# Kernel tuning notes

Measured on AMD Instinct MI355X. Metric: run time of the kernel, lower is better.

## Reference

```python
import jax, jax.numpy as jnp
import numpy as np
import math

N_HEADS = 16
D_EMBED = 1024
D_HEAD = D_EMBED // N_HEADS


def setup_inputs() -> dict:
    key = jax.random.key(0)
    ks = jax.random.split(key, 5)
    B, T = 4, 2048
    x = jax.random.normal(ks[0], (B, T, D_EMBED), dtype=jnp.float32)
    s_in = 1.0 / math.sqrt(D_EMBED)
    W_in = jax.random.normal(ks[1], (3 * D_EMBED, D_EMBED), dtype=jnp.float32) * s_in
    b_in = jax.random.normal(ks[2], (3 * D_EMBED,), dtype=jnp.float32) * s_in
    W_out = jax.random.normal(ks[3], (D_EMBED, D_EMBED), dtype=jnp.float32) * s_in
    b_out = jax.random.normal(ks[4], (D_EMBED,), dtype=jnp.float32) * s_in
    return {"x": x, "W_in": W_in, "b_in": b_in, "W_out": W_out, "b_out": b_out,
            "causal_mask": 1}


def reference(x, W_in, b_in, W_out, b_out, causal_mask):
    B, T, C = x.shape
    # in_proj: x @ W_in^T + b_in -> (B,T,3C), chunk into q,k,v
    qkv = jnp.einsum('btc,ec->bte', x, W_in) + b_in
    q, k, v = jnp.split(qkv, 3, axis=-1)
    # (B,T,H,Dh) -> (B,H,T,Dh)
    def heads(t):
        return t.reshape(B, T, N_HEADS, D_HEAD).transpose(0, 2, 1, 3)
    q, k, v = heads(q), heads(k), heads(v)
    scores = jnp.einsum('bhqd,bhkd->bhqk', q, k) / math.sqrt(D_HEAD)
    if causal_mask:
        mask = jnp.triu(jnp.ones((T, T), dtype=bool), k=1)  # True above diagonal
        scores = jnp.where(mask, -jnp.inf, scores)
    attn = jax.nn.softmax(scores, axis=-1)
    out = jnp.einsum('bhqk,bhkd->bhqd', attn, v)
    out = out.transpose(0, 2, 1, 3).reshape(B, T, C)
    out = jnp.einsum('btc,oc->bto', out, W_out) + b_out
    return out
```

## Files before the change

kernel.cpp:

```cpp
#include <hip/hip_runtime.h>
#include <hip/hip_bf16.h>

#define T_SEQ 2048
#define D_EMB 1024
#define NH    16
#define DH    64
#define NB    4
#define MROWS (NB * T_SEQ)
#define QKVN  (3 * D_EMB)

typedef __attribute__((ext_vector_type(8))) short bf16x8;
typedef __attribute__((ext_vector_type(4))) float f32x4;

__device__ __forceinline__ unsigned short f2bf(float f) {
  __hip_bfloat16 h = __float2bfloat16(f);
  return __builtin_bit_cast(unsigned short, h);
}

__device__ __forceinline__ void gload_lds16(const void* g, void* lds) {
  __builtin_amdgcn_global_load_lds(
      (const __attribute__((address_space(1))) void*)g,
      (__attribute__((address_space(3))) void*)lds, 16, 0, 0);
}

__global__ __launch_bounds__(256) void cvt_kernel(const float* __restrict__ in,
                                                  unsigned short* __restrict__ out,
                                                  int n4) {
  for (int i = blockIdx.x * 256 + threadIdx.x; i < n4; i += gridDim.x * 256) {
    const float4 v = reinterpret_cast<const float4*>(in)[i];
    ushort4 o;
    o.x = f2bf(v.x); o.y = f2bf(v.y); o.z = f2bf(v.z); o.w = f2bf(v.w);
    reinterpret_cast<ushort4*>(out)[i] = o;
  }
}

template <int OUT_BF16>
__global__ __launch_bounds__(256) void gemm_bt(const unsigned short* __restrict__ A,
                                               const unsigned short* __restrict__ Bt,
                                               const float* __restrict__ bias,
                                               void* __restrict__ Cout,
                                               int M, int N, int K) {
  __shared__ __align__(16) unsigned short As[128 * 32];
  __shared__ __align__(16) unsigned short Bs[128 * 32];

  const int tid = threadIdx.x;
  const int w  = tid >> 6;
  const int l  = tid & 63;
  const int lr = l & 15;
  const int lk = (l >> 4) * 8;
  const int bm = blockIdx.y * 128;
  const int bn = blockIdx.x * 128;
  const int wr = (w >> 1) * 64;
  const int wc = (w & 1) * 64;

  f32x4 acc[4][4];
#pragma unroll
  for (int i = 0; i < 4; ++i)
#pragma unroll
    for (int j = 0; j < 4; ++j) acc[i][j] = (f32x4){0.f, 0.f, 0.f, 0.f};

  const int srow = l >> 2;
  const int sk   = (l & 3) * 8;
  const unsigned short* Ab = A + (size_t)(bm + w * 32 + srow) * K + sk;
  const unsigned short* Bb = Bt + (size_t)(bn + w * 32 + srow) * K + sk;

  for (int kt = 0; kt < K; kt += 32) {
    gload_lds16(Ab + kt,                  &As[(w * 32 + 0) * 32]);
    gload_lds16(Ab + kt + (size_t)16 * K, &As[(w * 32 + 16) * 32]);
    gload_lds16(Bb + kt,                  &Bs[(w * 32 + 0) * 32]);
    gload_lds16(Bb + kt + (size_t)16 * K, &Bs[(w * 32 + 16) * 32]);
    __syncthreads();

    bf16x8 a[4], b[4];
#pragma unroll
    for (int mi = 0; mi < 4; ++mi)
      a[mi] = *reinterpret_cast<const bf16x8*>(&As[(wr + mi * 16 + lr) * 32 + lk]);
#pragma unroll
    for (int ni = 0; ni < 4; ++ni)
      b[ni] = *reinterpret_cast<const bf16x8*>(&Bs[(wc + ni * 16 + lr) * 32 + lk]);
#pragma unroll
    for (int mi = 0; mi < 4; ++mi)
#pragma unroll
      for (int ni = 0; ni < 4; ++ni)
        acc[mi][ni] = __builtin_amdgcn_mfma_f32_16x16x32_bf16(a[mi], b[ni], acc[mi][ni], 0, 0, 0);
    __syncthreads();
  }

  const int lg = l >> 4;
#pragma unroll
  for (int mi = 0; mi < 4; ++mi)
#pragma unroll
    for (int ni = 0; ni < 4; ++ni)
#pragma unroll
      for (int i = 0; i < 4; ++i) {
        const int row = bm + wr + mi * 16 + lg * 4 + i;
        const int col = bn + wc + ni * 16 + lr;
        const float v = acc[mi][ni][i] + bias[col];
        if (OUT_BF16)
          ((unsigned short*)Cout)[(size_t)row * N + col] = f2bf(v);
        else
          ((float*)Cout)[(size_t)row * N + col] = v;
      }
}

__global__ __launch_bounds__(512, 4) void attn_fwd(const unsigned short* __restrict__ qkv,
                                                   unsigned short* __restrict__ attn_out,
                                                   const int* __restrict__ causal_flag) {
  __shared__ __align__(16) unsigned short Ks[64 * 64];
  __shared__ __align__(16) unsigned short Vt[64 * 64];
  __shared__ __align__(16) unsigned short Ps[8][16 * 64];

  const int tid = threadIdx.x;
  const int w  = tid >> 6;
  const int l  = tid & 63;
  const int lr = l & 15;
  const int lg = l >> 4;
  const int lk = lg * 8;
  const int bx = blockIdx.x;
  const int bh = blockIdx.y;
  const int b  = bh >> 4;
  const int h  = bh & 15;
  const int causal = causal_flag[0];

  const unsigned short* Qp = qkv + (size_t)(b * T_SEQ) * QKVN + h * DH;
  const unsigned short* Kp = Qp + D_EMB;
  const unsigned short* Vp = Qp + 2 * D_EMB;

  for (int qq = 0; qq < 2; ++qq) {
    const int qt = qq ? (15 - bx) : bx;
    const int qbase = qt * 128;
    const int wrow0 = qbase + w * 16;

    bf16x8 qf[2];
#pragma unroll
    for (int ks = 0; ks < 2; ++ks) {
      bf16x8 v = *reinterpret_cast<const bf16x8*>(
          Qp + (size_t)(wrow0 + lr) * QKVN + ks * 32 + lk);
#pragma unroll
      for (int j = 0; j < 8; ++j) {
        const float f = __builtin_bit_cast(float, ((unsigned)(unsigned short)v[j]) << 16)
                        * 0.180336879f;
        v[j] = (short)(__builtin_bit_cast(unsigned, f) >> 16);
      }
      qf[ks] = v;
    }

    f32x4 oacc[4];
    float mrow = -INFINITY, lsum = 0.f;
#pragma unroll
    for (int di = 0; di < 4; ++di) oacc[di] = (f32x4){0.f, 0.f, 0.f, 0.f};

    const int nt = causal ? (qt * 2 + 2) : (T_SEQ / 64);

    for (int kb = 0; kb < nt; ++kb) {
      const int kbase = kb * 64;
      {
        const int cj = (l & 7) ^ (l >> 3);
        gload_lds16(Kp + (size_t)(kbase + w * 8 + (l >> 3)) * QKVN + cj * 8,
                    &Ks[(w * 8) * 64]);
      }
      {
        const int k  = tid & 63;
        const int d0 = (tid >> 6) * 8;
        bf16x8 v = *reinterpret_cast<const bf16x8*>(Vp + (size_t)(kbase + k) * QKVN + d0);
#pragma unroll
        for (int j = 0; j < 8; ++j)
          Vt[(d0 + j) * 64 + (k ^ (j << 3))] = ((unsigned short*)&v)[j];
      }
      __syncthreads();

      const bool live = !causal || (kbase <= wrow0 + 15);
      if (live) {
        f32x4 s[4];
#pragma unroll
        for (int ni = 0; ni < 4; ++ni) s[ni] = (f32x4){0.f, 0.f, 0.f, 0.f};
#pragma unroll
        for (int ks = 0; ks < 2; ++ks) {
          bf16x8 kf[4];
#pragma unroll
          for (int ni = 0; ni < 4; ++ni) {
            const int R = ni * 16 + lr;
            kf[ni] = *reinterpret_cast<const bf16x8*>(
                &Ks[R * 64 + (((ks * 4 + lg) ^ (lr & 7)) << 3)]);
          }
#pragma unroll
          for (int ni = 0; ni < 4; ++ni)
            s[ni] = __builtin_amdgcn_mfma_f32_16x16x32_bf16(kf[ni], qf[ks], s[ni], 0, 0, 0);
        }

        const bool mm = causal && (kbase + 63 > wrow0);
        const int qrow_rel = wrow0 + lr - kbase;
        float rmax = -INFINITY;
#pragma unroll
        for (int ni = 0; ni < 4; ++ni)
#pragma unroll
          for (int i = 0; i < 4; ++i) {
            float v = s[ni][i];
            if (mm && (ni * 16 + lg * 4 + i > qrow_rel)) v = -INFINITY;
            s[ni][i] = v;
            rmax = fmaxf(rmax, v);
          }
        rmax = fmaxf(rmax, __shfl_xor(rmax, 16));
        rmax = fmaxf(rmax, __shfl_xor(rmax, 32));
        const float mnew = fmaxf(mrow, rmax);
        const float alpha = exp2f(mrow - mnew);
        mrow = mnew;
        float psum = 0.f;
#pragma unroll
        for (int ni = 0; ni < 4; ++ni)
#pragma unroll
          for (int i = 0; i < 4; ++i) {
            const float p = exp2f(s[ni][i] - mnew);
            s[ni][i] = p;
            psum += p;
          }
        psum += __shfl_xor(psum, 16);
        psum += __shfl_xor(psum, 32);
        lsum = lsum * alpha + psum;

#pragma unroll
        for (int i = 0; i < 4; ++i) {
          const float a_bc = __shfl(alpha, (l & 48) | (lg * 4 + i));
#pragma unroll
          for (int di = 0; di < 4; ++di) oacc[di][i] *= a_bc;
        }

#pragma unroll
        for (int ni = 0; ni < 4; ++ni) {
          const unsigned lo = (unsigned)f2bf(s[ni][0]) | ((unsigned)f2bf(s[ni][1]) << 16);
          const unsigned hi = (unsigned)f2bf(s[ni][2]) | ((unsigned)f2bf(s[ni][3]) << 16);
          const int chunk = (ni * 2 + (lg >> 1)) ^ (lr & 7);
          uint2* dst = reinterpret_cast<uint2*>(
              reinterpret_cast<char*>(&Ps[w][0]) + lr * 128 + chunk * 16 + (lg & 1) * 8);
          *dst = make_uint2(lo, hi);
        }

#pragma unroll
        for (int ks2 = 0; ks2 < 2; ++ks2) {
          bf16x8 pf, vf[4];
          pf = *reinterpret_cast<const bf16x8*>(
              &Ps[w][lr * 64 + (((ks2 * 4 + lg) ^ (lr & 7)) << 3)]);
#pragma unroll
          for (int di = 0; di < 4; ++di) {
            const int R = di * 16 + lr;
            vf[di] = *reinterpret_cast<const bf16x8*>(
                &Vt[R * 64 + (((ks2 * 4 + lg) ^ (lr & 7)) << 3)]);
          }
#pragma unroll
          for (int di = 0; di < 4; ++di)
            oacc[di] = __builtin_amdgcn_mfma_f32_16x16x32_bf16(pf, vf[di], oacc[di], 0, 0, 0);
        }
      }
      __syncthreads();
    }

#pragma unroll
    for (int i = 0; i < 4; ++i) {
      const float ls = __shfl(lsum, (l & 48) | (lg * 4 + i));
      const float inv = 1.0f / ls;
#pragma unroll
      for (int di = 0; di < 4; ++di) {
        const int q = wrow0 + lg * 4 + i;
        const int d = di * 16 + lr;
        attn_out[(size_t)(b * T_SEQ + q) * D_EMB + h * DH + d] =
            f2bf(oacc[di][i] * inv);
      }
    }
  }
}

extern "C" void kernel_launch(void* const* d_in, const int* in_sizes, int n_in,
                              void* d_out, int out_size, void* d_ws, size_t ws_size,
                              hipStream_t stream) {
  const float* x     = (const float*)d_in[0];
  const float* W_in  = (const float*)d_in[1];
  const float* b_in  = (const float*)d_in[2];
  const float* W_out = (const float*)d_in[3];
  const float* b_out = (const float*)d_in[4];
  const int*   causal = (const int*)d_in[5];
  float* out = (float*)d_out;

  char* ws = (char*)d_ws;
  unsigned short* x_bf    = (unsigned short*)(ws);
  unsigned short* win_bf  = (unsigned short*)(ws + 16777216);
  unsigned short* wout_bf = (unsigned short*)(ws + 23068672);
  unsigned short* qkv     = (unsigned short*)(ws + 25165824);
  unsigned short* attn    = (unsigned short*)(ws + 75497472);

  cvt_kernel<<<2048, 256, 0, stream>>>(x, x_bf, (MROWS * D_EMB) / 4);
  cvt_kernel<<<2048, 256, 0, stream>>>(W_in, win_bf, (QKVN * D_EMB) / 4);
  cvt_kernel<<<1024, 256, 0, stream>>>(W_out, wout_bf, (D_EMB * D_EMB) / 4);

  gemm_bt<1><<<dim3(QKVN / 128, MROWS / 128), 256, 0, stream>>>(
      x_bf, win_bf, b_in, qkv, MROWS, QKVN, D_EMB);

  attn_fwd<<<dim3(8, NB * NH), 512, 0, stream>>>(qkv, attn, causal);

  gemm_bt<0><<<dim3(D_EMB / 128, MROWS / 128), 256, 0, stream>>>(
      attn, wout_bf, b_out, out, MROWS, D_EMB, D_EMB);
}
```

Measured before the change: 299.2 us.

## Pre-transpose V in a separate kernel and widen GEMM K-tile with swizzled LDS

Adds a transposeV kernel that writes V head-major and transposed into the workspace, so attention can stage V tiles with direct global-to-LDS loads instead of scalar transposing stores in its inner loop. The GEMM now uses a K-tile of 64 with XOR-swizzled LDS layout, which halves the number of barriers per K. It also remaps workgroups through a swizzle for better L2 locality. The trade-off is an extra kernel launch plus a round trip of V through memory, and twice the LDS per GEMM block.

```diff
diff --git a/kernel.cpp b/kernel.cpp
--- a/kernel.cpp
+++ b/kernel.cpp
@@ -34,22 +34,57 @@
   }
 }
 
+__global__ __launch_bounds__(256) void transposeV(const unsigned short* __restrict__ qkv,
+                                                  unsigned short* __restrict__ vt) {
+  __shared__ __align__(16) unsigned short Lt[64 * 72];
+  const int tid = threadIdx.x;
+  const int t0 = blockIdx.x * 64;
+  const int bh = blockIdx.y;
+  const int b  = bh >> 4;
+  const int h  = bh & 15;
+  const unsigned short* src = qkv + (size_t)(b * T_SEQ) * QKVN + 2 * D_EMB + h * DH;
+#pragma unroll
+  for (int g = 0; g < 2; ++g) {
+    const int r = (tid >> 3) + g * 32;
+    const int c = tid & 7;
+    bf16x8 v = *reinterpret_cast<const bf16x8*>(src + (size_t)(t0 + r) * QKVN + c * 8);
+    *reinterpret_cast<bf16x8*>(reinterpret_cast<char*>(Lt) + r * 144 + c * 16) = v;
+  }
+  __syncthreads();
+#pragma unroll
+  for (int g = 0; g < 2; ++g) {
+    const int d  = (tid >> 3) + g * 32;
+    const int tc = tid & 7;
+    bf16x8 o;
+#pragma unroll
+    for (int j = 0; j < 8; ++j)
+      ((unsigned short*)&o)[j] = Lt[(tc * 8 + j) * 72 + d];
+    *reinterpret_cast<bf16x8*>(vt + ((size_t)bh * 64 + d) * T_SEQ + t0 + tc * 8) = o;
+  }
+}
+
 template <int OUT_BF16>
 __global__ __launch_bounds__(256) void gemm_bt(const unsigned short* __restrict__ A,
                                                const unsigned short* __restrict__ Bt,
                                                const float* __restrict__ bias,
                                                void* __restrict__ Cout,
                                                int M, int N, int K) {
-  __shared__ __align__(16) unsigned short As[128 * 32];
-  __shared__ __align__(16) unsigned short Bs[128 * 32];
+  __shared__ __align__(16) unsigned short As[128 * 64];
+  __shared__ __align__(16) unsigned short Bs[128 * 64];
 
   const int tid = threadIdx.x;
   const int w  = tid >> 6;
   const int l  = tid & 63;
   const int lr = l & 15;
-  const int lk = (l >> 4) * 8;
-  const int bm = blockIdx.y * 128;
-  const int bn = blockIdx.x * 128;
+  const int lg = l >> 4;
+
+  const int gx   = gridDim.x;
+  const int nwg  = gx * gridDim.y;
+  const int orig = blockIdx.y * gx + blockIdx.x;
+  const int swz  = (orig & 7) * (nwg >> 3) + (orig >> 3);
+  const int bm = (swz / gx) * 128;
+  const int bn = (swz % gx) * 128;
+
   const int wr = (w >> 1) * 64;
   const int wc = (w & 1) * 64;
 
@@ -59,34 +94,42 @@
 #pragma unroll
     for (int j = 0; j < 4; ++j) acc[i][j] = (f32x4){0.f, 0.f, 0.f, 0.f};
 
-  const int srow = l >> 2;
-  const int sk   = (l & 3) * 8;
-  const unsigned short* Ab = A + (size_t)(bm + w * 32 + srow) * K + sk;
-  const unsigned short* Bb = Bt + (size_t)(bn + w * 32 + srow) * K + sk;
-
-  for (int kt = 0; kt < K; kt += 32) {
-    gload_lds16(Ab + kt,                  &As[(w * 32 + 0) * 32]);
-    gload_lds16(Ab + kt + (size_t)16 * K, &As[(w * 32 + 16) * 32]);
-    gload_lds16(Bb + kt,                  &Bs[(w * 32 + 0) * 32]);
-    gload_lds16(Bb + kt + (size_t)16 * K, &Bs[(w * 32 + 16) * 32]);
+  const int cj = (l & 7) ^ (l >> 3);
+  const unsigned short* Ab = A + (size_t)(bm + w * 32 + (l >> 3)) * K + cj * 8;
+  const unsigned short* Bb = Bt + (size_t)(bn + w * 32 + (l >> 3)) * K + cj * 8;
+
+  for (int kt = 0; kt < K; kt += 64) {
+#pragma unroll
+    for (int i = 0; i < 4; ++i) {
+      gload_lds16(Ab + kt + (size_t)(i * 8) * K, &As[(w * 32 + i * 8) * 64]);
+      gload_lds16(Bb + kt + (size_t)(i * 8) * K, &Bs[(w * 32 + i * 8) * 64]);
+    }
     __syncthreads();
 
-    bf16x8 a[4], b[4];
-#pragma unroll
-    for (int mi = 0; mi < 4; ++mi)
-      a[mi] = *reinterpret_cast<const bf16x8*>(&As[(wr + mi * 16 + lr) * 32 + lk]);
-#pragma unroll
-    for (int ni = 0; ni < 4; ++ni)
-      b[ni] = *reinterpret_cast<const bf16x8*>(&Bs[(wc + ni * 16 + lr) * 32 + lk]);
-#pragma unroll
-    for (int mi = 0; mi < 4; ++mi)
-#pragma unroll
-      for (int ni = 0; ni < 4; ++ni)
-        acc[mi][ni] = __builtin_amdgcn_mfma_f32_16x16x32_bf16(a[mi], b[ni], acc[mi][ni], 0, 0, 0);
+#pragma unroll
+    for (int kk = 0; kk < 2; ++kk) {
+      bf16x8 a[4], b[4];
+#pragma unroll
+      for (int mi = 0; mi < 4; ++mi) {
+        const int R = wr + mi * 16 + lr;
+        a[mi] = *reinterpret_cast<const bf16x8*>(
+            &As[R * 64 + (((kk * 4 + lg) ^ (lr & 7)) << 3)]);
+      }
+#pragma unroll
+      for (int ni = 0; ni < 4; ++ni) {
+        const int R = wc + ni * 16 + lr;
+        b[ni] = *reinterpret_cast<const bf16x8*>(
+            &Bs[R * 64 + (((kk * 4 + lg) ^ (lr & 7)) << 3)]);
+      }
+#pragma unroll
+      for (int mi = 0; mi < 4; ++mi)
+#pragma unroll
+        for (int ni = 0; ni < 4; ++ni)
+          acc[mi][ni] = __builtin_amdgcn_mfma_f32_16x16x32_bf16(a[mi], b[ni], acc[mi][ni], 0, 0, 0);
+    }
     __syncthreads();
   }
 
-  const int lg = l >> 4;
 #pragma unroll
   for (int mi = 0; mi < 4; ++mi)
 #pragma unroll
@@ -104,6 +147,7 @@
 }
 
 __global__ __launch_bounds__(512, 4) void attn_fwd(const unsigned short* __restrict__ qkv,
+                                                   const unsigned short* __restrict__ vt,
                                                    unsigned short* __restrict__ attn_out,
                                                    const int* __restrict__ causal_flag) {
   __shared__ __align__(16) unsigned short Ks[64 * 64];
@@ -122,9 +166,12 @@
   const int h  = bh & 15;
   const int causal = causal_flag[0];
 
-  const unsigned short* Qp = qkv + (size_t)(b * T_SEQ) * QKVN + h * DH;
-  const unsigned short* Kp = Qp + D_EMB;
-  const unsigned short* Vp = Qp + 2 * D_EMB;
+  const unsigned short* Qp  = qkv + (size_t)(b * T_SEQ) * QKVN + h * DH;
+  const unsigned short* Kp  = Qp + D_EMB;
+  const unsigned short* Vtp = vt + (size_t)bh * 64 * T_SEQ;
+
+  const int scj = (l & 7) ^ (l >> 3);
+  const int srr = l >> 3;
 
   for (int qq = 0; qq < 2; ++qq) {
     const int qt = qq ? (15 - bx) : bx;
@@ -154,19 +201,10 @@
 
     for (int kb = 0; kb < nt; ++kb) {
       const int kbase = kb * 64;
-      {
-        const int cj = (l & 7) ^ (l >> 3);
-        gload_lds16(Kp + (size_t)(kbase + w * 8 + (l >> 3)) * QKVN + cj * 8,
-                    &Ks[(w * 8) * 64]);
-      }
-      {
-        const int k  = tid & 63;
-        const int d0 = (tid >> 6) * 8;
-        bf16x8 v = *reinterpret_cast<const bf16x8*>(Vp + (size_t)(kbase + k) * QKVN + d0);
-#pragma unroll
-        for (int j = 0; j < 8; ++j)
-          Vt[(d0 + j) * 64 + (k ^ (j << 3))] = ((unsigned short*)&v)[j];
-      }
+      gload_lds16(Kp + (size_t)(kbase + w * 8 + srr) * QKVN + scj * 8,
+                  &Ks[(w * 8) * 64]);
+      gload_lds16(Vtp + (size_t)(w * 8 + srr) * T_SEQ + kbase + scj * 8,
+                  &Vt[(w * 8) * 64]);
       __syncthreads();
 
       const bool live = !causal || (kbase <= wrow0 + 15);
@@ -282,6 +320,7 @@
 
   char* ws = (char*)d_ws;
   unsigned short* x_bf    = (unsigned short*)(ws);
+  unsigned short* vt      = (unsigned short*)(ws);
   unsigned short* win_bf  = (unsigned short*)(ws + 16777216);
   unsigned short* wout_bf = (unsigned short*)(ws + 23068672);
   unsigned short* qkv     = (unsigned short*)(ws + 25165824);
@@ -294,7 +333,9 @@
   gemm_bt<1><<<dim3(QKVN / 128, MROWS / 128), 256, 0, stream>>>(
       x_bf, win_bf, b_in, qkv, MROWS, QKVN, D_EMB);
 
-  attn_fwd<<<dim3(8, NB * NH), 512, 0, stream>>>(qkv, attn, causal);
+  transposeV<<<dim3(T_SEQ / 64, NB * NH), 256, 0, stream>>>(qkv, vt);
+
+  attn_fwd<<<dim3(8, NB * NH), 512, 0, stream>>>(qkv, vt, attn, causal);
 
   gemm_bt<0><<<dim3(D_EMB / 128, MROWS / 128), 256, 0, stream>>>(
       attn, wout_bf, b_out, out, MROWS, D_EMB, D_EMB);
```

Measured after the change: 296.3 us. About the same (-1.0%).
